# Performance work log

Measured on AMD Instinct MI355X. Metric: run time of the kernel, lower is better.

The kernel has to match this reference:

```python
import jax, jax.numpy as jnp
import numpy as np

N = 50000   # num_nodes
T = 24      # window_size
H = 64      # hidden_dim
HOR = 12    # horizon
E = 1600000 # num edges


def setup_inputs() -> dict:
    key = jax.random.key(0)
    ks = jax.random.split(key, 12)
    s = 1.0 / np.sqrt(H)
    u = lambda k, shape: jax.random.uniform(k, shape, jnp.float32, -s, s)
    return {
        "x": jax.random.normal(ks[0], (N, T), jnp.float32),
        "edge_index": jax.random.randint(ks[1], (2, E), 0, N, dtype=jnp.int32),
        "w_ih": u(ks[2], (3 * H, 1)),
        "w_hh": u(ks[3], (3 * H, H)),
        "b_ih": u(ks[4], (3 * H,)),
        "b_hh": u(ks[5], (3 * H,)),
        "gc1_w": u(ks[6], (H, H)),
        "gc1_b": u(ks[7], (H,)),
        "gc2_w": u(ks[8], (H, H)),
        "gc2_b": u(ks[9], (H,)),
        "fc_w": u(ks[10], (HOR, H)),
        "fc_b": u(ks[11], (HOR,)),
    }


def _gru_last(x, w_ih, w_hh, b_ih, b_hh):
    # x: [N, T] scalar-per-step input (input_size=1). Returns final hidden [N, H].
    h0 = jnp.zeros((x.shape[0], H), x.dtype)

    def step(h, xt):  # xt: [N]
        gi = xt[:, None] * w_ih[:, 0][None, :] + b_ih   # [N, 3H]
        gh = h @ w_hh.T + b_hh                          # [N, 3H]
        i_r, i_z, i_n = jnp.split(gi, 3, axis=-1)
        h_r, h_z, h_n = jnp.split(gh, 3, axis=-1)
        r = jax.nn.sigmoid(i_r + h_r)
        z = jax.nn.sigmoid(i_z + h_z)
        n = jnp.tanh(i_n + r * h_n)
        h = (1.0 - z) * n + z * h
        return h, None

    hT, _ = jax.lax.scan(step, h0, x.T)  # scan over time axis
    return hT


def _gcn_norm(edge_index, n):
    # PyG GCNConv: add self loops, symmetric D^-1/2 (A+I) D^-1/2 normalization.
    loops = jnp.arange(n, dtype=edge_index.dtype)
    src = jnp.concatenate([edge_index[0], loops])
    dst = jnp.concatenate([edge_index[1], loops])
    deg = jax.ops.segment_sum(jnp.ones(src.shape, jnp.float32), dst, num_segments=n)
    dinv = jnp.where(deg > 0, jax.lax.rsqrt(jnp.maximum(deg, 1e-12)), 0.0)
    return src, dst, dinv[src] * dinv[dst]


def _gcn(h, src, dst, norm, W, b, n):
    hw = h @ W.T                      # [N, H] linear transform first
    msg = hw[src] * norm[:, None]     # gather + edge weighting
    return jax.ops.segment_sum(msg, dst, num_segments=n) + b


def reference(x, edge_index, w_ih, w_hh, b_ih, b_hh, gc1_w, gc1_b, gc2_w, gc2_b, fc_w, fc_b):
    n = x.shape[0]
    h = _gru_last(x, w_ih, w_hh, b_ih, b_hh)            # [N, H] last GRU output
    src, dst, norm = _gcn_norm(edge_index, n)
    h = jax.nn.relu(_gcn(h, src, dst, norm, gc1_w, gc1_b, n))
    h = jax.nn.relu(_gcn(h, src, dst, norm, gc2_w, gc2_b, n))
    return h @ fc_w.T + fc_b                            # [N, HOR]
```

## Files before the change

kernel.cpp:

```cpp
#include <hip/hip_runtime.h>

#define NN 50000
#define TT 24
#define HH 64
#define HORZ 12
#define EE 1600000

#define GP 256
#define EP (EE / GP)
#define BK 784
#define NBG (BK * GP)
#define SCB (NBG / 512)

typedef __attribute__((ext_vector_type(8))) _Float16 f16x8;
typedef __attribute__((ext_vector_type(4))) float f32x4;

__device__ __forceinline__ float sigm(float x) {
  return __builtin_amdgcn_rcpf(1.f + __expf(-x));
}
__device__ __forceinline__ float tanh_f(float x) {
  return 1.f - 2.f * __builtin_amdgcn_rcpf(1.f + __expf(2.f * x));
}

__global__ void build_frags_kernel(const float* __restrict__ whh, const float* __restrict__ g1,
                                   const float* __restrict__ g2, const float* __restrict__ fcw,
                                   _Float16* __restrict__ frag) {
  int idx = blockIdx.x * 256 + threadIdx.x;
  if (idx >= 21504) return;
  const float* W;
  int rows, li;
  if (idx < 12288) { W = whh; rows = 192; li = idx; }
  else if (idx < 16384) { W = g1; rows = 64; li = idx - 12288; }
  else if (idx < 20480) { W = g2; rows = 64; li = idx - 16384; }
  else { W = fcw; rows = HORZ; li = idx - 20480; }
  int j = li & 7;
  int l = (li >> 3) & 63;
  int kf = (li >> 9) & 1;
  int nf = li >> 10;
  int col = 16 * nf + (l & 15);
  int k = 32 * kf + 8 * (l >> 4) + j;
  frag[idx] = (col < rows) ? (_Float16)W[col * 64 + k] : (_Float16)0.f;
}

__global__ __launch_bounds__(256, 6) void gru_kernel(
    const float* __restrict__ x, const float* __restrict__ w_ih,
    const float* __restrict__ b_ih, const float* __restrict__ b_hh,
    const _Float16* __restrict__ wfrag, _Float16* __restrict__ hout) {
  __shared__ __align__(16) _Float16 sh[2][16][72];

  const int tid = threadIdx.x;
  const int lane = tid & 63;
  const int w = tid >> 6;
  const int c = lane & 15;
  const int q = lane >> 4;
  const int d = 16 * w + c;

  f16x8 Br0 = *(const f16x8*)&wfrag[(((w)*2 + 0) * 64 + lane) * 8];
  f16x8 Br1 = *(const f16x8*)&wfrag[(((w)*2 + 1) * 64 + lane) * 8];
  f16x8 Bz0 = *(const f16x8*)&wfrag[(((4 + w) * 2 + 0) * 64 + lane) * 8];
  f16x8 Bz1 = *(const f16x8*)&wfrag[(((4 + w) * 2 + 1) * 64 + lane) * 8];
  f16x8 Bn0 = *(const f16x8*)&wfrag[(((8 + w) * 2 + 0) * 64 + lane) * 8];
  f16x8 Bn1 = *(const f16x8*)&wfrag[(((8 + w) * 2 + 1) * 64 + lane) * 8];

  const float wir = w_ih[d], wiz = w_ih[64 + d], win = w_ih[128 + d];
  const float arb = b_ih[d] + b_hh[d];
  const float azb = b_ih[64 + d] + b_hh[64 + d];
  const float bin = b_ih[128 + d];
  const float bhn = b_hh[128 + d];

  const int base = blockIdx.x * 16;
  const float* xb = x + base * TT;

  float hreg[4] = {0.f, 0.f, 0.f, 0.f};

#pragma unroll 1
  for (int t = 0; t < TT; ++t) {
    f32x4 ar = (f32x4){arb, arb, arb, arb};
    f32x4 az = (f32x4){azb, azb, azb, azb};
    f32x4 an = (f32x4){bhn, bhn, bhn, bhn};
    if (t > 0) {
      const _Float16* S = &sh[(t & 1) ^ 1][0][0];
      f16x8 a0 = *(const f16x8*)&S[c * 72 + 8 * q];
      f16x8 a1 = *(const f16x8*)&S[c * 72 + 32 + 8 * q];
      ar = __builtin_amdgcn_mfma_f32_16x16x32_f16(a0, Br0, ar, 0, 0, 0);
      az = __builtin_amdgcn_mfma_f32_16x16x32_f16(a0, Bz0, az, 0, 0, 0);
      an = __builtin_amdgcn_mfma_f32_16x16x32_f16(a0, Bn0, an, 0, 0, 0);
      ar = __builtin_amdgcn_mfma_f32_16x16x32_f16(a1, Br1, ar, 0, 0, 0);
      az = __builtin_amdgcn_mfma_f32_16x16x32_f16(a1, Bz1, az, 0, 0, 0);
      an = __builtin_amdgcn_mfma_f32_16x16x32_f16(a1, Bn1, an, 0, 0, 0);
    }
#pragma unroll
    for (int r = 0; r < 4; ++r) {
      float xt = xb[(4 * q + r) * TT + t];
      float rg = sigm(xt * wir + ar[r]);
      float zg = sigm(xt * wiz + az[r]);
      float nn = tanh_f(rg * an[r] + (xt * win + bin));
      float hn = nn + zg * (hreg[r] - nn);
      hreg[r] = hn;
      sh[t & 1][4 * q + r][d] = (_Float16)hn;
    }
    __syncthreads();
  }

#pragma unroll
  for (int r = 0; r < 4; ++r) hout[(base + 4 * q + r) * 64 + d] = (_Float16)hreg[r];
}

__global__ __launch_bounds__(256) void p1_hist_kernel(const int* __restrict__ dst,
                                                      int* __restrict__ hist) {
  __shared__ int h[BK];
  int tid = threadIdx.x, g = blockIdx.x;
  for (int b = tid; b < BK; b += 256) h[b] = 0;
  __syncthreads();
  int e0 = g * EP;
  for (int i = tid; i < EP; i += 256) atomicAdd(&h[dst[e0 + i] >> 6], 1);
  __syncthreads();
  for (int b = tid; b < BK; b += 256) hist[b * GP + g] = h[b];
}

__global__ void scanA_kernel(const int* __restrict__ v, int* __restrict__ part) {
  __shared__ int s[512];
  int i = blockIdx.x * 512 + threadIdx.x;
  s[threadIdx.x] = v[i];
  __syncthreads();
  for (int off = 256; off > 0; off >>= 1) {
    if (threadIdx.x < off) s[threadIdx.x] += s[threadIdx.x + off];
    __syncthreads();
  }
  if (threadIdx.x == 0) part[blockIdx.x] = s[0];
}

__global__ void scanB_kernel(int* __restrict__ part) {
  __shared__ int s[512];
  int t = threadIdx.x;
  int v = (t < SCB) ? part[t] : 0;
  s[t] = v;
  __syncthreads();
  for (int off = 1; off < 512; off <<= 1) {
    int a = s[t];
    int b = (t >= off) ? s[t - off] : 0;
    __syncthreads();
    s[t] = a + b;
    __syncthreads();
  }
  if (t < SCB) part[t] = s[t] - v;
}

__global__ void scanC_kernel(int* __restrict__ cellbase, const int* __restrict__ part) {
  __shared__ int s[2][512];
  int tid = threadIdx.x;
  int i = blockIdx.x * 512 + tid;
  int x = cellbase[i];
  s[0][tid] = x;
  __syncthreads();
  int cur = 0;
  for (int off = 1; off < 512; off <<= 1) {
    int nxt = cur ^ 1;
    int val = s[cur][tid] + ((tid >= off) ? s[cur][tid - off] : 0);
    s[nxt][tid] = val;
    __syncthreads();
    cur = nxt;
  }
  cellbase[i] = part[blockIdx.x] + s[cur][tid] - x;
  if (i == 0) cellbase[NBG] = EE;
}

__global__ __launch_bounds__(256) void p2_scatter_kernel(
    const int* __restrict__ src, const int* __restrict__ dst,
    const int* __restrict__ cellbase, unsigned int* __restrict__ rec) {
  __shared__ int cur[BK];
  int tid = threadIdx.x, g = blockIdx.x;
  for (int b = tid; b < BK; b += 256) cur[b] = cellbase[b * GP + g];
  __syncthreads();
  int e0 = g * EP;
  for (int i = tid; i < EP; i += 256) {
    int e = e0 + i;
    int d = dst[e];
    int s = src[e];
    int p = atomicAdd(&cur[d >> 6], 1);
    rec[p] = ((unsigned)(d & 63) << 16) | (unsigned)s;
  }
}

__global__ __launch_bounds__(256) void sort2_kernel(
    const unsigned int* __restrict__ rec, const int* __restrict__ cellbase,
    unsigned short* __restrict__ csr, int* __restrict__ row_start,
    float* __restrict__ dinv) {
  __shared__ int cnt[64];
  __shared__ int cur[64];
  int b = blockIdx.x, tid = threadIdx.x;
  if (tid < 64) cnt[tid] = 0;
  __syncthreads();
  int e0 = cellbase[b * GP], e1 = cellbase[(b + 1) * GP];
  for (int e = e0 + tid; e < e1; e += 256) atomicAdd(&cnt[rec[e] >> 16], 1);
  __syncthreads();
  if (tid == 0) {
    int a = e0;
#pragma unroll
    for (int l = 0; l < 64; ++l) { int c = cnt[l]; cur[l] = a; a += c; }
  }
  __syncthreads();
  if (tid < 64) {
    int n = b * 64 + tid;
    if (n <= NN) row_start[n] = cur[tid];
    if (n < NN) dinv[n] = rsqrtf((float)(cnt[tid] + 1));
  }
  __syncthreads();
  for (int e = e0 + tid; e < e1; e += 256) {
    unsigned int r = rec[e];
    int p = atomicAdd(&cur[r >> 16], 1);
    csr[p] = (unsigned short)(r & 0xFFFFu);
  }
}

__global__ __launch_bounds__(256) void linear_mfma_kernel(
    const _Float16* __restrict__ hin, const _Float16* __restrict__ frag,
    const float* __restrict__ dinv, _Float16* __restrict__ out) {
  const int tid = threadIdx.x;
  const int lane = tid & 63;
  const int w = tid >> 6;
  const int c = lane & 15;
  const int q = lane >> 4;
  int n0 = blockIdx.x * 64 + w * 16;
  int nA = n0 + c;
  int nc = nA < NN ? nA : NN - 1;
  const _Float16* hp = hin + nc * 64;

  f16x8 a0 = *(const f16x8*)&hp[8 * q];
  f16x8 a1 = *(const f16x8*)&hp[32 + 8 * q];
  f32x4 acc[4];
#pragma unroll
  for (int nf = 0; nf < 4; ++nf) acc[nf] = (f32x4){0.f, 0.f, 0.f, 0.f};
#pragma unroll
  for (int nf = 0; nf < 4; ++nf) {
    f16x8 b0 = *(const f16x8*)&frag[((nf * 2 + 0) * 64 + lane) * 8];
    acc[nf] = __builtin_amdgcn_mfma_f32_16x16x32_f16(a0, b0, acc[nf], 0, 0, 0);
  }
#pragma unroll
  for (int nf = 0; nf < 4; ++nf) {
    f16x8 b1 = *(const f16x8*)&frag[((nf * 2 + 1) * 64 + lane) * 8];
    acc[nf] = __builtin_amdgcn_mfma_f32_16x16x32_f16(a1, b1, acc[nf], 0, 0, 0);
  }
#pragma unroll
  for (int r = 0; r < 4; ++r) {
    int n = n0 + 4 * q + r;
    if (n < NN) {
      float dn = dinv[n];
#pragma unroll
      for (int nf = 0; nf < 4; ++nf)
        out[n * 64 + c + 16 * nf] = (_Float16)(acc[nf][r] * dn);
    }
  }
}

__global__ __launch_bounds__(256) void agg_kernel(
    const _Float16* __restrict__ hwp, const float* __restrict__ dinv,
    const int* __restrict__ row_start, const unsigned short* __restrict__ csr,
    const float* __restrict__ bias, _Float16* __restrict__ out) {
  int wid = blockIdx.x * 4 + (threadIdx.x >> 6);
  int lane = threadIdx.x & 63;
  if (wid >= NN) return;
  int e0 = row_start[wid], e1 = row_start[wid + 1];
  float a0 = (float)hwp[wid * 64 + lane];
  float a1 = 0.f, a2 = 0.f, a3 = 0.f;
  int e = e0;
  for (; e < e1 && (e & 7); ++e) a0 += (float)hwp[(int)csr[e] * 64 + lane];
  for (; e + 8 <= e1; e += 8) {
    uint4 pk = *(const uint4*)&csr[e];
    int s0 = pk.x & 0xFFFF, s1 = pk.x >> 16;
    int s2 = pk.y & 0xFFFF, s3 = pk.y >> 16;
    int s4 = pk.z & 0xFFFF, s5 = pk.z >> 16;
    int s6 = pk.w & 0xFFFF, s7 = pk.w >> 16;
    a0 += (float)hwp[s0 * 64 + lane];
    a1 += (float)hwp[s1 * 64 + lane];
    a2 += (float)hwp[s2 * 64 + lane];
    a3 += (float)hwp[s3 * 64 + lane];
    a0 += (float)hwp[s4 * 64 + lane];
    a1 += (float)hwp[s5 * 64 + lane];
    a2 += (float)hwp[s6 * 64 + lane];
    a3 += (float)hwp[s7 * 64 + lane];
  }
  for (; e < e1; ++e) a0 += (float)hwp[(int)csr[e] * 64 + lane];
  float v = (a0 + a1 + a2 + a3) * dinv[wid] + bias[lane];
  out[wid * 64 + lane] = (_Float16)(v > 0.f ? v : 0.f);
}

__global__ __launch_bounds__(256) void fc_mfma_kernel(
    const _Float16* __restrict__ hin, const _Float16* __restrict__ frag,
    const float* __restrict__ bias, float* __restrict__ out) {
  const int tid = threadIdx.x;
  const int lane = tid & 63;
  const int w = tid >> 6;
  const int c = lane & 15;
  const int q = lane >> 4;
  int n0 = blockIdx.x * 64 + w * 16;
  int nA = n0 + c;
  int nc = nA < NN ? nA : NN - 1;
  const _Float16* hp = hin + nc * 64;

  f16x8 a0 = *(const f16x8*)&hp[8 * q];
  f16x8 a1 = *(const f16x8*)&hp[32 + 8 * q];
  float bc = (c < HORZ) ? bias[c] : 0.f;
  f32x4 acc = (f32x4){bc, bc, bc, bc};
  f16x8 b0 = *(const f16x8*)&frag[(0 * 64 + lane) * 8];
  f16x8 b1 = *(const f16x8*)&frag[(1 * 64 + lane) * 8];
  acc = __builtin_amdgcn_mfma_f32_16x16x32_f16(a0, b0, acc, 0, 0, 0);
  acc = __builtin_amdgcn_mfma_f32_16x16x32_f16(a1, b1, acc, 0, 0, 0);
  if (c < HORZ) {
#pragma unroll
    for (int r = 0; r < 4; ++r) {
      int n = n0 + 4 * q + r;
      if (n < NN) out[n * HORZ + c] = acc[r];
    }
  }
}

extern "C" void kernel_launch(void* const* d_in, const int* in_sizes, int n_in,
                              void* d_out, int out_size, void* d_ws, size_t ws_size,
                              hipStream_t stream) {
  (void)in_sizes; (void)n_in; (void)out_size; (void)ws_size;
  const float* x = (const float*)d_in[0];
  const int* edge_index = (const int*)d_in[1];
  const float* w_ih = (const float*)d_in[2];
  const float* w_hh = (const float*)d_in[3];
  const float* b_ih = (const float*)d_in[4];
  const float* b_hh = (const float*)d_in[5];
  const float* gc1_w = (const float*)d_in[6];
  const float* gc1_b = (const float*)d_in[7];
  const float* gc2_w = (const float*)d_in[8];
  const float* gc2_b = (const float*)d_in[9];
  const float* fc_w = (const float*)d_in[10];
  const float* fc_b = (const float*)d_in[11];
  float* out = (float*)d_out;

  char* ws = (char*)d_ws;
  _Float16* wfrag = (_Float16*)ws;
  _Float16* l1f = wfrag + 12288;
  _Float16* l2f = l1f + 4096;
  _Float16* fcf = l2f + 4096;
  _Float16* hbuf = (_Float16*)(ws + 43008);
  _Float16* hw = hbuf + NN * 64;
  float* dinv = (float*)(hw + NN * 64);
  int* row_start = (int*)(dinv + NN);
  int* cellbase = row_start + 50240;
  int* part = cellbase + NBG + 4;
  unsigned int* rec = (unsigned int*)(part + 512);
  unsigned short* csr = (unsigned short*)(rec + EE);

  const int* esrc = edge_index;
  const int* edst = edge_index + EE;

  build_frags_kernel<<<84, 256, 0, stream>>>(w_hh, gc1_w, gc2_w, fc_w, wfrag);
  gru_kernel<<<NN / 16, 256, 0, stream>>>(x, w_ih, b_ih, b_hh, wfrag, hbuf);

  p1_hist_kernel<<<GP, 256, 0, stream>>>(edst, cellbase);
  scanA_kernel<<<SCB, 512, 0, stream>>>(cellbase, part);
  scanB_kernel<<<1, 512, 0, stream>>>(part);
  scanC_kernel<<<SCB, 512, 0, stream>>>(cellbase, part);
  p2_scatter_kernel<<<GP, 256, 0, stream>>>(esrc, edst, cellbase, rec);
  sort2_kernel<<<BK, 256, 0, stream>>>(rec, cellbase, csr, row_start, dinv);

  linear_mfma_kernel<<<(NN + 63) / 64, 256, 0, stream>>>(hbuf, l1f, dinv, hw);
  agg_kernel<<<(NN + 3) / 4, 256, 0, stream>>>(hw, dinv, row_start, csr, gc1_b, hbuf);
  linear_mfma_kernel<<<(NN + 63) / 64, 256, 0, stream>>>(hbuf, l2f, dinv, hw);
  agg_kernel<<<(NN + 3) / 4, 256, 0, stream>>>(hw, dinv, row_start, csr, gc2_b, hbuf);
  fc_mfma_kernel<<<(NN + 63) / 64, 256, 0, stream>>>(hbuf, fcf, fc_b, out);
}
```

Baseline: 259.7 us.

## Fuse GCN linear transforms into GRU and aggregation kernels

Moves the GRU launch after the CSR build so it can apply the first GCN linear transform and dinv scaling in its epilogue. It also folds the second linear layer and the final FC into the aggregation kernels through shared-memory MFMA tiles. The GRU block now handles two 16-node groups and stages x in LDS. This removes three launches and the intermediate hidden-state round trips through global memory, at the cost of serialising the GRU behind graph preprocessing and using larger 1024-thread aggregation blocks.

```diff
diff --git a/kernel.cpp b/kernel.cpp
--- a/kernel.cpp
+++ b/kernel.cpp
@@ -11,6 +11,7 @@
 #define BK 784
 #define NBG (BK * GP)
 #define SCB (NBG / 512)
+#define BKA ((NN + 63) / 64)
 
 typedef __attribute__((ext_vector_type(8))) _Float16 f16x8;
 typedef __attribute__((ext_vector_type(4))) float f32x4;
@@ -42,70 +43,6 @@
   frag[idx] = (col < rows) ? (_Float16)W[col * 64 + k] : (_Float16)0.f;
 }
 
-__global__ __launch_bounds__(256, 6) void gru_kernel(
-    const float* __restrict__ x, const float* __restrict__ w_ih,
-    const float* __restrict__ b_ih, const float* __restrict__ b_hh,
-    const _Float16* __restrict__ wfrag, _Float16* __restrict__ hout) {
-  __shared__ __align__(16) _Float16 sh[2][16][72];
-
-  const int tid = threadIdx.x;
-  const int lane = tid & 63;
-  const int w = tid >> 6;
-  const int c = lane & 15;
-  const int q = lane >> 4;
-  const int d = 16 * w + c;
-
-  f16x8 Br0 = *(const f16x8*)&wfrag[(((w)*2 + 0) * 64 + lane) * 8];
-  f16x8 Br1 = *(const f16x8*)&wfrag[(((w)*2 + 1) * 64 + lane) * 8];
-  f16x8 Bz0 = *(const f16x8*)&wfrag[(((4 + w) * 2 + 0) * 64 + lane) * 8];
-  f16x8 Bz1 = *(const f16x8*)&wfrag[(((4 + w) * 2 + 1) * 64 + lane) * 8];
-  f16x8 Bn0 = *(const f16x8*)&wfrag[(((8 + w) * 2 + 0) * 64 + lane) * 8];
-  f16x8 Bn1 = *(const f16x8*)&wfrag[(((8 + w) * 2 + 1) * 64 + lane) * 8];
-
-  const float wir = w_ih[d], wiz = w_ih[64 + d], win = w_ih[128 + d];
-  const float arb = b_ih[d] + b_hh[d];
-  const float azb = b_ih[64 + d] + b_hh[64 + d];
-  const float bin = b_ih[128 + d];
-  const float bhn = b_hh[128 + d];
-
-  const int base = blockIdx.x * 16;
-  const float* xb = x + base * TT;
-
-  float hreg[4] = {0.f, 0.f, 0.f, 0.f};
-
-#pragma unroll 1
-  for (int t = 0; t < TT; ++t) {
-    f32x4 ar = (f32x4){arb, arb, arb, arb};
-    f32x4 az = (f32x4){azb, azb, azb, azb};
-    f32x4 an = (f32x4){bhn, bhn, bhn, bhn};
-    if (t > 0) {
-      const _Float16* S = &sh[(t & 1) ^ 1][0][0];
-      f16x8 a0 = *(const f16x8*)&S[c * 72 + 8 * q];
-      f16x8 a1 = *(const f16x8*)&S[c * 72 + 32 + 8 * q];
-      ar = __builtin_amdgcn_mfma_f32_16x16x32_f16(a0, Br0, ar, 0, 0, 0);
-      az = __builtin_amdgcn_mfma_f32_16x16x32_f16(a0, Bz0, az, 0, 0, 0);
-      an = __builtin_amdgcn_mfma_f32_16x16x32_f16(a0, Bn0, an, 0, 0, 0);
-      ar = __builtin_amdgcn_mfma_f32_16x16x32_f16(a1, Br1, ar, 0, 0, 0);
-      az = __builtin_amdgcn_mfma_f32_16x16x32_f16(a1, Bz1, az, 0, 0, 0);
-      an = __builtin_amdgcn_mfma_f32_16x16x32_f16(a1, Bn1, an, 0, 0, 0);
-    }
-#pragma unroll
-    for (int r = 0; r < 4; ++r) {
-      float xt = xb[(4 * q + r) * TT + t];
-      float rg = sigm(xt * wir + ar[r]);
-      float zg = sigm(xt * wiz + az[r]);
-      float nn = tanh_f(rg * an[r] + (xt * win + bin));
-      float hn = nn + zg * (hreg[r] - nn);
-      hreg[r] = hn;
-      sh[t & 1][4 * q + r][d] = (_Float16)hn;
-    }
-    __syncthreads();
-  }
-
-#pragma unroll
-  for (int r = 0; r < 4; ++r) hout[(base + 4 * q + r) * 64 + d] = (_Float16)hreg[r];
-}
-
 __global__ __launch_bounds__(256) void p1_hist_kernel(const int* __restrict__ dst,
                                                       int* __restrict__ hist) {
   __shared__ int h[BK];
@@ -213,104 +150,210 @@
   }
 }
 
-__global__ __launch_bounds__(256) void linear_mfma_kernel(
-    const _Float16* __restrict__ hin, const _Float16* __restrict__ frag,
-    const float* __restrict__ dinv, _Float16* __restrict__ out) {
+__global__ __launch_bounds__(256, 4) void gru_kernel(
+    const float* __restrict__ x, const float* __restrict__ w_ih,
+    const float* __restrict__ b_ih, const float* __restrict__ b_hh,
+    const _Float16* __restrict__ wfrag, const _Float16* __restrict__ l1f,
+    const float* __restrict__ dinv, _Float16* __restrict__ hw) {
+  __shared__ __align__(16) _Float16 sh[2][2][16][72];
+  __shared__ __align__(16) float xs[2][TT][16];
+
   const int tid = threadIdx.x;
   const int lane = tid & 63;
   const int w = tid >> 6;
   const int c = lane & 15;
   const int q = lane >> 4;
-  int n0 = blockIdx.x * 64 + w * 16;
-  int nA = n0 + c;
-  int nc = nA < NN ? nA : NN - 1;
-  const _Float16* hp = hin + nc * 64;
-
-  f16x8 a0 = *(const f16x8*)&hp[8 * q];
-  f16x8 a1 = *(const f16x8*)&hp[32 + 8 * q];
-  f32x4 acc[4];
-#pragma unroll
-  for (int nf = 0; nf < 4; ++nf) acc[nf] = (f32x4){0.f, 0.f, 0.f, 0.f};
-#pragma unroll
-  for (int nf = 0; nf < 4; ++nf) {
-    f16x8 b0 = *(const f16x8*)&frag[((nf * 2 + 0) * 64 + lane) * 8];
-    acc[nf] = __builtin_amdgcn_mfma_f32_16x16x32_f16(a0, b0, acc[nf], 0, 0, 0);
-  }
-#pragma unroll
-  for (int nf = 0; nf < 4; ++nf) {
-    f16x8 b1 = *(const f16x8*)&frag[((nf * 2 + 1) * 64 + lane) * 8];
-    acc[nf] = __builtin_amdgcn_mfma_f32_16x16x32_f16(a1, b1, acc[nf], 0, 0, 0);
-  }
-#pragma unroll
-  for (int r = 0; r < 4; ++r) {
-    int n = n0 + 4 * q + r;
-    if (n < NN) {
-      float dn = dinv[n];
-#pragma unroll
-      for (int nf = 0; nf < 4; ++nf)
-        out[n * 64 + c + 16 * nf] = (_Float16)(acc[nf][r] * dn);
+  const int d = 16 * w + c;
+
+  f16x8 Br0 = *(const f16x8*)&wfrag[(((w)*2 + 0) * 64 + lane) * 8];
+  f16x8 Br1 = *(const f16x8*)&wfrag[(((w)*2 + 1) * 64 + lane) * 8];
+  f16x8 Bz0 = *(const f16x8*)&wfrag[(((4 + w) * 2 + 0) * 64 + lane) * 8];
+  f16x8 Bz1 = *(const f16x8*)&wfrag[(((4 + w) * 2 + 1) * 64 + lane) * 8];
+  f16x8 Bn0 = *(const f16x8*)&wfrag[(((8 + w) * 2 + 0) * 64 + lane) * 8];
+  f16x8 Bn1 = *(const f16x8*)&wfrag[(((8 + w) * 2 + 1) * 64 + lane) * 8];
+
+  const float wir = w_ih[d], wiz = w_ih[64 + d], win = w_ih[128 + d];
+  const float arb = b_ih[d] + b_hh[d];
+  const float azb = b_ih[64 + d] + b_hh[64 + d];
+  const float bin = b_ih[128 + d];
+  const float bhn = b_hh[128 + d];
+
+  const int base = blockIdx.x * 32;
+
+  for (int i = tid; i < 32 * TT; i += 256) {
+    int nl = i / TT;
+    int t = i - nl * TT;
+    int node = base + nl;
+    xs[nl >> 4][t][nl & 15] = (node < NN) ? x[node * TT + t] : 0.f;
+  }
+  __syncthreads();
+
+  float hreg[2][4];
+#pragma unroll
+  for (int g = 0; g < 2; ++g)
+#pragma unroll
+    for (int r = 0; r < 4; ++r) hreg[g][r] = 0.f;
+
+#pragma unroll 1
+  for (int t = 0; t < TT; ++t) {
+#pragma unroll
+    for (int g = 0; g < 2; ++g) {
+      f32x4 ar = (f32x4){arb, arb, arb, arb};
+      f32x4 az = (f32x4){azb, azb, azb, azb};
+      f32x4 an = (f32x4){bhn, bhn, bhn, bhn};
+      if (t > 0) {
+        const _Float16* S = &sh[(t & 1) ^ 1][g][0][0];
+        f16x8 a0 = *(const f16x8*)&S[c * 72 + 8 * q];
+        f16x8 a1 = *(const f16x8*)&S[c * 72 + 32 + 8 * q];
+        ar = __builtin_amdgcn_mfma_f32_16x16x32_f16(a0, Br0, ar, 0, 0, 0);
+        az = __builtin_amdgcn_mfma_f32_16x16x32_f16(a0, Bz0, az, 0, 0, 0);
+        an = __builtin_amdgcn_mfma_f32_16x16x32_f16(a0, Bn0, an, 0, 0, 0);
+        ar = __builtin_amdgcn_mfma_f32_16x16x32_f16(a1, Br1, ar, 0, 0, 0);
+        az = __builtin_amdgcn_mfma_f32_16x16x32_f16(a1, Bz1, az, 0, 0, 0);
+        an = __builtin_amdgcn_mfma_f32_16x16x32_f16(a1, Bn1, an, 0, 0, 0);
+      }
+      float4 xt = *(const float4*)&xs[g][t][4 * q];
+      float xv[4] = {xt.x, xt.y, xt.z, xt.w};
+#pragma unroll
+      for (int r = 0; r < 4; ++r) {
+        float rg = sigm(xv[r] * wir + ar[r]);
+        float zg = sigm(xv[r] * wiz + az[r]);
+        float nn = tanh_f(rg * an[r] + (xv[r] * win + bin));
+        float hn = nn + zg * (hreg[g][r] - nn);
+        hreg[g][r] = hn;
+        sh[t & 1][g][4 * q + r][d] = (_Float16)hn;
+      }
     }
-  }
-}
-
-__global__ __launch_bounds__(256) void agg_kernel(
+    __syncthreads();
+  }
+
+  f16x8 L0 = *(const f16x8*)&l1f[((w * 2 + 0) * 64 + lane) * 8];
+  f16x8 L1 = *(const f16x8*)&l1f[((w * 2 + 1) * 64 + lane) * 8];
+#pragma unroll
+  for (int g = 0; g < 2; ++g) {
+    const _Float16* S = &sh[1][g][0][0];
+    f16x8 a0 = *(const f16x8*)&S[c * 72 + 8 * q];
+    f16x8 a1 = *(const f16x8*)&S[c * 72 + 32 + 8 * q];
+    f32x4 acc = (f32x4){0.f, 0.f, 0.f, 0.f};
+    acc = __builtin_amdgcn_mfma_f32_16x16x32_f16(a0, L0, acc, 0, 0, 0);
+    acc = __builtin_amdgcn_mfma_f32_16x16x32_f16(a1, L1, acc, 0, 0, 0);
+#pragma unroll
+    for (int r = 0; r < 4; ++r) {
+      int n = base + 16 * g + 4 * q + r;
+      if (n < NN) hw[n * 64 + d] = (_Float16)(acc[r] * dinv[n]);
+    }
+  }
+}
+
+__global__ __launch_bounds__(1024, 4) void agg_lin_kernel(
     const _Float16* __restrict__ hwp, const float* __restrict__ dinv,
     const int* __restrict__ row_start, const unsigned short* __restrict__ csr,
-    const float* __restrict__ bias, _Float16* __restrict__ out) {
-  int wid = blockIdx.x * 4 + (threadIdx.x >> 6);
-  int lane = threadIdx.x & 63;
-  if (wid >= NN) return;
-  int e0 = row_start[wid], e1 = row_start[wid + 1];
-  float a0 = (float)hwp[wid * 64 + lane];
-  float a1 = 0.f, a2 = 0.f, a3 = 0.f;
-  int e = e0;
-  for (; e < e1 && (e & 7); ++e) a0 += (float)hwp[(int)csr[e] * 64 + lane];
-  for (; e + 8 <= e1; e += 8) {
-    uint4 pk = *(const uint4*)&csr[e];
-    int s0 = pk.x & 0xFFFF, s1 = pk.x >> 16;
-    int s2 = pk.y & 0xFFFF, s3 = pk.y >> 16;
-    int s4 = pk.z & 0xFFFF, s5 = pk.z >> 16;
-    int s6 = pk.w & 0xFFFF, s7 = pk.w >> 16;
-    a0 += (float)hwp[s0 * 64 + lane];
-    a1 += (float)hwp[s1 * 64 + lane];
-    a2 += (float)hwp[s2 * 64 + lane];
-    a3 += (float)hwp[s3 * 64 + lane];
-    a0 += (float)hwp[s4 * 64 + lane];
-    a1 += (float)hwp[s5 * 64 + lane];
-    a2 += (float)hwp[s6 * 64 + lane];
-    a3 += (float)hwp[s7 * 64 + lane];
-  }
-  for (; e < e1; ++e) a0 += (float)hwp[(int)csr[e] * 64 + lane];
-  float v = (a0 + a1 + a2 + a3) * dinv[wid] + bias[lane];
-  out[wid * 64 + lane] = (_Float16)(v > 0.f ? v : 0.f);
-}
-
-__global__ __launch_bounds__(256) void fc_mfma_kernel(
-    const _Float16* __restrict__ hin, const _Float16* __restrict__ frag,
-    const float* __restrict__ bias, float* __restrict__ out) {
-  const int tid = threadIdx.x;
-  const int lane = tid & 63;
-  const int w = tid >> 6;
-  const int c = lane & 15;
-  const int q = lane >> 4;
-  int n0 = blockIdx.x * 64 + w * 16;
-  int nA = n0 + c;
-  int nc = nA < NN ? nA : NN - 1;
-  const _Float16* hp = hin + nc * 64;
-
-  f16x8 a0 = *(const f16x8*)&hp[8 * q];
-  f16x8 a1 = *(const f16x8*)&hp[32 + 8 * q];
-  float bc = (c < HORZ) ? bias[c] : 0.f;
-  f32x4 acc = (f32x4){bc, bc, bc, bc};
-  f16x8 b0 = *(const f16x8*)&frag[(0 * 64 + lane) * 8];
-  f16x8 b1 = *(const f16x8*)&frag[(1 * 64 + lane) * 8];
-  acc = __builtin_amdgcn_mfma_f32_16x16x32_f16(a0, b0, acc, 0, 0, 0);
-  acc = __builtin_amdgcn_mfma_f32_16x16x32_f16(a1, b1, acc, 0, 0, 0);
-  if (c < HORZ) {
-#pragma unroll
-    for (int r = 0; r < 4; ++r) {
-      int n = n0 + 4 * q + r;
-      if (n < NN) out[n * HORZ + c] = acc[r];
+    const float* __restrict__ bias, const _Float16* __restrict__ l2f,
+    _Float16* __restrict__ out) {
+  __shared__ __align__(16) _Float16 h1[64][72];
+  int tid = threadIdx.x, b = blockIdx.x;
+  int wv = tid >> 6, lane = tid & 63;
+  float bl = bias[lane];
+#pragma unroll 1
+  for (int k = 0; k < 4; ++k) {
+    int row = wv * 4 + k;
+    int n = b * 64 + row;
+    float v = 0.f;
+    if (n < NN) {
+      int e0 = row_start[n], e1 = row_start[n + 1];
+      float a0 = (float)hwp[n * 64 + lane];
+      float a1 = 0.f, a2 = 0.f, a3 = 0.f;
+      int e = e0;
+      for (; e < e1 && (e & 7); ++e) a0 += (float)hwp[(int)csr[e] * 64 + lane];
+      for (; e + 8 <= e1; e += 8) {
+        uint4 pk = *(const uint4*)&csr[e];
+        a0 += (float)hwp[(pk.x & 0xFFFF) * 64 + lane];
+        a1 += (float)hwp[(pk.x >> 16) * 64 + lane];
+        a2 += (float)hwp[(pk.y & 0xFFFF) * 64 + lane];
+        a3 += (float)hwp[(pk.y >> 16) * 64 + lane];
+        a0 += (float)hwp[(pk.z & 0xFFFF) * 64 + lane];
+        a1 += (float)hwp[(pk.z >> 16) * 64 + lane];
+        a2 += (float)hwp[(pk.w & 0xFFFF) * 64 + lane];
+        a3 += (float)hwp[(pk.w >> 16) * 64 + lane];
+      }
+      for (; e < e1; ++e) a0 += (float)hwp[(int)csr[e] * 64 + lane];
+      v = (a0 + a1 + a2 + a3) * dinv[n] + bl;
+      v = v > 0.f ? v : 0.f;
+    }
+    h1[row][lane] = (_Float16)v;
+  }
+  __syncthreads();
+  int g = wv >> 2, wq = wv & 3;
+  int c = lane & 15, q = lane >> 4;
+  f16x8 B0 = *(const f16x8*)&l2f[((wq * 2 + 0) * 64 + lane) * 8];
+  f16x8 B1 = *(const f16x8*)&l2f[((wq * 2 + 1) * 64 + lane) * 8];
+  f16x8 a0 = *(const f16x8*)&h1[16 * g + c][8 * q];
+  f16x8 a1 = *(const f16x8*)&h1[16 * g + c][32 + 8 * q];
+  f32x4 acc = (f32x4){0.f, 0.f, 0.f, 0.f};
+  acc = __builtin_amdgcn_mfma_f32_16x16x32_f16(a0, B0, acc, 0, 0, 0);
+  acc = __builtin_amdgcn_mfma_f32_16x16x32_f16(a1, B1, acc, 0, 0, 0);
+#pragma unroll
+  for (int r = 0; r < 4; ++r) {
+    int n = b * 64 + 16 * g + 4 * q + r;
+    if (n < NN) out[n * 64 + 16 * wq + c] = (_Float16)(acc[r] * dinv[n]);
+  }
+}
+
+__global__ __launch_bounds__(1024, 4) void agg_fc_kernel(
+    const _Float16* __restrict__ hwp, const float* __restrict__ dinv,
+    const int* __restrict__ row_start, const unsigned short* __restrict__ csr,
+    const float* __restrict__ bias, const _Float16* __restrict__ fcf,
+    const float* __restrict__ fcb, float* __restrict__ out) {
+  __shared__ __align__(16) _Float16 h1[64][72];
+  int tid = threadIdx.x, b = blockIdx.x;
+  int wv = tid >> 6, lane = tid & 63;
+  float bl = bias[lane];
+#pragma unroll 1
+  for (int k = 0; k < 4; ++k) {
+    int row = wv * 4 + k;
+    int n = b * 64 + row;
+    float v = 0.f;
+    if (n < NN) {
+      int e0 = row_start[n], e1 = row_start[n + 1];
+      float a0 = (float)hwp[n * 64 + lane];
+      float a1 = 0.f, a2 = 0.f, a3 = 0.f;
+      int e = e0;
+      for (; e < e1 && (e & 7); ++e) a0 += (float)hwp[(int)csr[e] * 64 + lane];
+      for (; e + 8 <= e1; e += 8) {
+        uint4 pk = *(const uint4*)&csr[e];
+        a0 += (float)hwp[(pk.x & 0xFFFF) * 64 + lane];
+        a1 += (float)hwp[(pk.x >> 16) * 64 + lane];
+        a2 += (float)hwp[(pk.y & 0xFFFF) * 64 + lane];
+        a3 += (float)hwp[(pk.y >> 16) * 64 + lane];
+        a0 += (float)hwp[(pk.z & 0xFFFF) * 64 + lane];
+        a1 += (float)hwp[(pk.z >> 16) * 64 + lane];
+        a2 += (float)hwp[(pk.w & 0xFFFF) * 64 + lane];
+        a3 += (float)hwp[(pk.w >> 16) * 64 + lane];
+      }
+      for (; e < e1; ++e) a0 += (float)hwp[(int)csr[e] * 64 + lane];
+      v = (a0 + a1 + a2 + a3) * dinv[n] + bl;
+      v = v > 0.f ? v : 0.f;
+    }
+    h1[row][lane] = (_Float16)v;
+  }
+  __syncthreads();
+  if (wv < 4) {
+    int g = wv;
+    int c = lane & 15, q = lane >> 4;
+    f16x8 B0 = *(const f16x8*)&fcf[(0 * 64 + lane) * 8];
+    f16x8 B1 = *(const f16x8*)&fcf[(1 * 64 + lane) * 8];
+    f16x8 a0 = *(const f16x8*)&h1[16 * g + c][8 * q];
+    f16x8 a1 = *(const f16x8*)&h1[16 * g + c][32 + 8 * q];
+    float bc = (c < HORZ) ? fcb[c] : 0.f;
+    f32x4 acc = (f32x4){bc, bc, bc, bc};
+    acc = __builtin_amdgcn_mfma_f32_16x16x32_f16(a0, B0, acc, 0, 0, 0);
+    acc = __builtin_amdgcn_mfma_f32_16x16x32_f16(a1, B1, acc, 0, 0, 0);
+    if (c < HORZ) {
+#pragma unroll
+      for (int r = 0; r < 4; ++r) {
+        int n = b * 64 + 16 * g + 4 * q + r;
+        if (n < NN) out[n * HORZ + c] = acc[r];
+      }
     }
   }
 }
@@ -338,9 +381,9 @@
   _Float16* l1f = wfrag + 12288;
   _Float16* l2f = l1f + 4096;
   _Float16* fcf = l2f + 4096;
-  _Float16* hbuf = (_Float16*)(ws + 43008);
-  _Float16* hw = hbuf + NN * 64;
-  float* dinv = (float*)(hw + NN * 64);
+  _Float16* hw1 = (_Float16*)(ws + 43008);
+  _Float16* hw2 = hw1 + NN * 64;
+  float* dinv = (float*)(hw2 + NN * 64);
   int* row_start = (int*)(dinv + NN);
   int* cellbase = row_start + 50240;
   int* part = cellbase + NBG + 4;
@@ -351,8 +394,6 @@
   const int* edst = edge_index + EE;
 
   build_frags_kernel<<<84, 256, 0, stream>>>(w_hh, gc1_w, gc2_w, fc_w, wfrag);
-  gru_kernel<<<NN / 16, 256, 0, stream>>>(x, w_ih, b_ih, b_hh, wfrag, hbuf);
-
   p1_hist_kernel<<<GP, 256, 0, stream>>>(edst, cellbase);
   scanA_kernel<<<SCB, 512, 0, stream>>>(cellbase, part);
   scanB_kernel<<<1, 512, 0, stream>>>(part);
@@ -360,9 +401,7 @@
   p2_scatter_kernel<<<GP, 256, 0, stream>>>(esrc, edst, cellbase, rec);
   sort2_kernel<<<BK, 256, 0, stream>>>(rec, cellbase, csr, row_start, dinv);
 
-  linear_mfma_kernel<<<(NN + 63) / 64, 256, 0, stream>>>(hbuf, l1f, dinv, hw);
-  agg_kernel<<<(NN + 3) / 4, 256, 0, stream>>>(hw, dinv, row_start, csr, gc1_b, hbuf);
-  linear_mfma_kernel<<<(NN + 63) / 64, 256, 0, stream>>>(hbuf, l2f, dinv, hw);
-  agg_kernel<<<(NN + 3) / 4, 256, 0, stream>>>(hw, dinv, row_start, csr, gc2_b, hbuf);
-  fc_mfma_kernel<<<(NN + 63) / 64, 256, 0, stream>>>(hbuf, fcf, fc_b, out);
-}
+  gru_kernel<<<(NN + 31) / 32, 256, 0, stream>>>(x, w_ih, b_ih, b_hh, wfrag, l1f, dinv, hw1);
+  agg_lin_kernel<<<BKA, 1024, 0, stream>>>(hw1, dinv, row_start, csr, gc1_b, l2f, hw2);
+  agg_fc_kernel<<<BKA, 1024, 0, stream>>>(hw2, dinv, row_start, csr, gc2_b, fcf, fc_b, out);
+}
```

Result: no change. 263.9 us (+1.6%).
